# Performance work log

Hardware: AMD Instinct MI355X
Metric: run time of the kernel (lower is better)

The kernel has to match this reference:

```python
import jax, jax.numpy as jnp
import numpy as np
import math

B, N, C = 4, 8192, 384
H = 6
D = C // H  # head_dim = 64


def setup_inputs() -> dict:
    key = jax.random.key(0)
    ks = jax.random.split(key, 9)
    s = 1.0 / math.sqrt(D)
    x = jax.random.normal(ks[0], (B, N, C), dtype=jnp.float32)
    Wq = jax.random.normal(ks[1], (H, D, D), dtype=jnp.float32) * s
    bq = jax.random.normal(ks[2], (H, D), dtype=jnp.float32) * 0.01
    Wk = jax.random.normal(ks[3], (H, D, D), dtype=jnp.float32) * s
    bk = jax.random.normal(ks[4], (H, D), dtype=jnp.float32) * 0.01
    Wv = jax.random.normal(ks[5], (H, D, D), dtype=jnp.float32) * s
    bv = jax.random.normal(ks[6], (H, D), dtype=jnp.float32) * 0.01
    Wp = jax.random.normal(ks[7], (C, C), dtype=jnp.float32) * (1.0 / math.sqrt(C))
    bp = jax.random.normal(ks[8], (C,), dtype=jnp.float32) * 0.01
    return {"x": x, "Wq": Wq, "bq": bq, "Wk": Wk, "bk": bk,
            "Wv": Wv, "bv": bv, "Wp": Wp, "bp": bp}


def reference(x, Wq, bq, Wk, bk, Wv, bv, Wp, bp):
    b, n, c = x.shape
    # [B, H, N, D]
    xh = x.reshape(b, n, H, D).transpose(0, 2, 1, 3)
    # Batched per-head projections (replaces the Python loop of per-head Linears)
    q = jnp.einsum('bhnd,hde->bhne', xh, Wq) + bq[:, None, :]
    k = jnp.einsum('bhnd,hde->bhne', xh, Wk) + bk[:, None, :]
    v = jnp.einsum('bhnd,hde->bhne', xh, Wv) + bv[:, None, :]
    q = jax.nn.softmax(q, axis=-1)          # over feature dim
    k = jax.nn.softmax(k, axis=-2)          # over sequence dim
    v = v * (1.0 / math.sqrt(D))
    kv = jnp.einsum('bhnd,bhne->bhde', k, v)   # [B,H,D,D] context
    out = jnp.einsum('bhnd,bhde->bhne', q, kv) # [B,H,N,D]
    out = out.transpose(0, 2, 1, 3).reshape(b, n, c)
    return out @ Wp.T + bp
```

## Files before the change

### kernel.cpp

```cpp
#include <hip/hip_runtime.h>
#include <hip/hip_bf16.h>


#define B 4
#define N 8192
#define C 384
#define H 6
#define D 64
#define BH (B * H)
#define BN (B * N)

typedef __attribute__((ext_vector_type(8))) short short8;
typedef __attribute__((ext_vector_type(4))) float f32x4;

__device__ inline unsigned short f2bf(float f) {
    unsigned int u = __float_as_uint(f);
    unsigned int r = (u + 0x7fff + ((u >> 16) & 1)) >> 16;
    return (unsigned short)r;
}
__device__ inline float bf2f(unsigned short h) {
    return __uint_as_float(((unsigned int)h) << 16);
}

__global__ void wprep(const float* __restrict__ Wq, const float* __restrict__ Wk,
                      const float* __restrict__ Wv,
                      unsigned short* __restrict__ Whi, unsigned short* __restrict__ Wlo)
{
    __shared__ float tmp[64][65];
    const int m = blockIdx.x / H;
    const int h = blockIdx.x % H;
    const float* in = (m == 0 ? Wq : m == 1 ? Wk : Wv) + h * 64 * 64;
    const int t = threadIdx.x;
    for (int d = 0; d < 64; ++d) tmp[d][t] = in[d * 64 + t];
    __syncthreads();
    const size_t base = ((size_t)(m * H + h)) * 64 * 64;
    for (int e = 0; e < 64; ++e) {
        float v = tmp[t][e];
        unsigned short hb = f2bf(v);
        Whi[base + e * 64 + t] = hb;
        Wlo[base + e * 64 + t] = f2bf(v - bf2f(hb));
    }
}

__global__ __launch_bounds__(256, 2) void proj_kernel(
    const float* __restrict__ x,
    const unsigned short* __restrict__ Whi, const unsigned short* __restrict__ Wlo,
    const float* __restrict__ bq, const float* __restrict__ bk,
    const float* __restrict__ bv,
    unsigned short* __restrict__ qout,
    float* __restrict__ kvraw, float* __restrict__ Sg)
{
    __shared__ __align__(16) char smem[81920];
    float* A_s = (float*)smem;
    unsigned short* W_s = (unsigned short*)(smem + 17408);
    unsigned short* qbuf = (unsigned short*)(smem + 72704);
    float* kvred = (float*)smem;
    float* sred  = (float*)(smem + 67584);

    const int blk = blockIdx.x;
    const int nb  = blk & 31;
    const int bh  = blk >> 5;
    const int b   = bh / H;
    const int h   = bh % H;
    const int n0  = nb * 256;
    const int t   = threadIdx.x;
    const int lane = t & 63;
    const int w   = t >> 6;
    const int lq  = lane & 15;
    const int qd  = lane >> 4;

    {
        const size_t hb64 = (size_t)h * 64 * 64;
        for (int id = t; id < 512; id += 256) {
            int e = id >> 3, j = id & 7;
            #pragma unroll
            for (int m = 0; m < 3; ++m) {
                const size_t src = ((size_t)m * H) * 64 * 64 + hb64 + e * 64 + 8 * j;
                *(uint4*)&W_s[(2 * m) * 4608 + e * 72 + 8 * j] = *(const uint4*)(Whi + src);
                *(uint4*)&W_s[(2 * m + 1) * 4608 + e * 72 + 8 * j] = *(const uint4*)(Wlo + src);
            }
        }
    }

    float bqv[4], bkv[4], bvv[4];
    #pragma unroll
    for (int j = 0; j < 4; ++j) {
        int col = j * 16 + lq;
        bqv[j] = bq[h * D + col];
        bkv[j] = bk[h * D + col];
        bvv[j] = bv[h * D + col];
    }

    f32x4 kvacc[4][4] = {};
    float sacc[4] = {};

    for (int sub = 0; sub < 4; ++sub) {
        __syncthreads();
        const int ns = n0 + sub * 64;
        for (int id = t; id < 1024; id += 256) {
            int r = id >> 4, j = id & 15;
            *(float4*)&A_s[r * 68 + 4 * j] =
                *(const float4*)(x + (size_t)(b * N + ns + r) * C + h * D + 4 * j);
        }
        __syncthreads();

        f32x4 acc[3][4] = {};
        #pragma unroll
        for (int ck = 0; ck < 2; ++ck) {
            const float* ap = A_s + (w * 16 + lq) * 68 + ck * 32 + qd * 8;
            float av[8];
            *(float4*)&av[0] = *(const float4*)ap;
            *(float4*)&av[4] = *(const float4*)(ap + 4);
            short8 ahi, alo;
            #pragma unroll
            for (int i = 0; i < 8; ++i) {
                unsigned short hb = f2bf(av[i]);
                ahi[i] = (short)hb;
                alo[i] = (short)f2bf(av[i] - bf2f(hb));
            }
            #pragma unroll
            for (int m = 0; m < 3; ++m) {
                #pragma unroll
                for (int j = 0; j < 4; ++j) {
                    const unsigned short* bp =
                        W_s + (2 * m) * 4608 + (j * 16 + lq) * 72 + ck * 32 + qd * 8;
                    short8 bhi = *(const short8*)bp;
                    short8 blo = *(const short8*)(bp + 4608);
                    acc[m][j] = __builtin_amdgcn_mfma_f32_16x16x32_bf16(alo, bhi, acc[m][j], 0, 0, 0);
                    acc[m][j] = __builtin_amdgcn_mfma_f32_16x16x32_bf16(ahi, blo, acc[m][j], 0, 0, 0);
                    acc[m][j] = __builtin_amdgcn_mfma_f32_16x16x32_bf16(ahi, bhi, acc[m][j], 0, 0, 0);
                }
            }
        }

        #pragma unroll
        for (int r = 0; r < 4; ++r) {
            const int row = w * 16 + qd * 4 + r;
            float qv[4];
            #pragma unroll
            for (int j = 0; j < 4; ++j) qv[j] = acc[0][j][r] + bqv[j];
            float mx = fmaxf(fmaxf(qv[0], qv[1]), fmaxf(qv[2], qv[3]));
            #pragma unroll
            for (int msk = 1; msk < 16; msk <<= 1) mx = fmaxf(mx, __shfl_xor(mx, msk));
            float e0 = __expf(qv[0] - mx), e1 = __expf(qv[1] - mx);
            float e2 = __expf(qv[2] - mx), e3 = __expf(qv[3] - mx);
            float s = e0 + e1 + e2 + e3;
            #pragma unroll
            for (int msk = 1; msk < 16; msk <<= 1) s += __shfl_xor(s, msk);
            float inv = 1.f / s;
            qbuf[row * 72 + 0 * 16 + lq] = f2bf(e0 * inv);
            qbuf[row * 72 + 1 * 16 + lq] = f2bf(e1 * inv);
            qbuf[row * 72 + 2 * 16 + lq] = f2bf(e2 * inv);
            qbuf[row * 72 + 3 * 16 + lq] = f2bf(e3 * inv);
        }

        short8 kfrag[4], vfrag[4];
        #pragma unroll
        for (int j = 0; j < 4; ++j) {
            float e0 = __expf(acc[1][j][0] + bkv[j]);
            float e1 = __expf(acc[1][j][1] + bkv[j]);
            float e2 = __expf(acc[1][j][2] + bkv[j]);
            float e3 = __expf(acc[1][j][3] + bkv[j]);
            float cs = e0 + e1 + e2 + e3;
            cs += __shfl_xor(cs, 16);
            cs += __shfl_xor(cs, 32);
            sacc[j] += cs;
            kfrag[j] = short8{(short)f2bf(e0), (short)f2bf(e1),
                              (short)f2bf(e2), (short)f2bf(e3), 0, 0, 0, 0};
            float v0 = (acc[2][j][0] + bvv[j]) * 0.125f;
            float v1 = (acc[2][j][1] + bvv[j]) * 0.125f;
            float v2 = (acc[2][j][2] + bvv[j]) * 0.125f;
            float v3 = (acc[2][j][3] + bvv[j]) * 0.125f;
            vfrag[j] = short8{(short)f2bf(v0), (short)f2bf(v1),
                              (short)f2bf(v2), (short)f2bf(v3), 0, 0, 0, 0};
        }
        #pragma unroll
        for (int i = 0; i < 4; ++i)
            #pragma unroll
            for (int j = 0; j < 4; ++j)
                kvacc[i][j] = __builtin_amdgcn_mfma_f32_16x16x32_bf16(
                    kfrag[i], vfrag[j], kvacc[i][j], 0, 0, 0);

        __syncthreads();
        for (int id = t; id < 512; id += 256) {
            int r = id >> 3, j = id & 7;
            *(uint4*)&qout[((size_t)bh * N + ns + r) * D + 8 * j] =
                *(uint4*)&qbuf[r * 72 + 8 * j];
        }
    }

    __syncthreads();

    #pragma unroll
    for (int i = 0; i < 4; ++i)
        #pragma unroll
        for (int j = 0; j < 4; ++j)
            #pragma unroll
            for (int r = 0; r < 4; ++r)
                kvred[w * 4224 + (i * 16 + qd * 4 + r) * 66 + j * 16 + lq] =
                    kvacc[i][j][r];
    if (qd == 0) {
        #pragma unroll
        for (int j = 0; j < 4; ++j) sred[w * 64 + j * 16 + lq] = sacc[j];
    }
    __syncthreads();

    for (int idx = t; idx < 4096; idx += 256) {
        int d = idx >> 6, e = idx & 63;
        float s = kvred[d * 66 + e] + kvred[4224 + d * 66 + e]
                + kvred[2 * 4224 + d * 66 + e] + kvred[3 * 4224 + d * 66 + e];
        atomicAdd(&kvraw[bh * 4096 + idx], s);
    }
    if (t < 64) {
        float s = sred[t] + sred[64 + t] + sred[128 + t] + sred[192 + t];
        atomicAdd(&Sg[bh * 64 + t], s);
    }
}

__global__ __launch_bounds__(256) void kw_kernel(
    const float* __restrict__ kvraw, const float* __restrict__ Sg,
    const float* __restrict__ Wp, unsigned short* __restrict__ KWT)
{
    __shared__ float kv_s[64 * 68];
    __shared__ float w_s[64 * 68];
    __shared__ float rS_s[64];
    const int bh = blockIdx.x / (C / 64);
    const int ct = blockIdx.x % (C / 64);
    const int b = bh / H, h = bh % H;
    const int c0 = ct * 64;
    const int t = threadIdx.x, dg = t >> 4, cg = t & 15;

    if (t < 64) rS_s[t] = 1.f / Sg[bh * 64 + t];
    __syncthreads();

    for (int i = t; i < 4096; i += 256) {
        int row = i >> 6, e = i & 63;
        kv_s[e * 68 + row] = kvraw[bh * (D * D) + row * 64 + e] * rS_s[row];
        w_s[e * 68 + row]  = Wp[(size_t)(c0 + row) * C + h * 64 + e];
    }
    __syncthreads();

    float acc[4][4] = {};
    for (int e = 0; e < 64; ++e) {
        float4 a = *(float4*)&kv_s[e * 68 + dg * 4];
        float4 w = *(float4*)&w_s[e * 68 + cg * 4];
        const float a4[4] = {a.x, a.y, a.z, a.w};
        const float w4[4] = {w.x, w.y, w.z, w.w};
        #pragma unroll
        for (int i = 0; i < 4; ++i)
            #pragma unroll
            for (int j = 0; j < 4; ++j) acc[i][j] += a4[i] * w4[j];
    }
    #pragma unroll
    for (int i = 0; i < 4; ++i)
        #pragma unroll
        for (int j = 0; j < 4; ++j) {
            int d = dg * 4 + i, c = c0 + cg * 4 + j;
            KWT[((size_t)b * C + c) * (H * D) + h * 64 + d] = f2bf(acc[i][j]);
        }
}

__global__ __launch_bounds__(256) void out_gemm(
    const unsigned short* __restrict__ q, const unsigned short* __restrict__ KWT,
    const float* __restrict__ bp, float* __restrict__ out)
{
    __shared__ __align__(16) unsigned short A_s[128 * 72];
    __shared__ __align__(16) unsigned short B_s[128 * 72];

    const int mt = blockIdx.x / (C / 128);
    const int ct = blockIdx.x % (C / 128);
    const int m0 = mt * 128, c0 = ct * 128;
    const int b  = m0 >> 13;
    const int n0 = m0 & (N - 1);
    const int t  = threadIdx.x;
    const int lane = t & 63;
    const int w  = t >> 6;
    const int wm = w >> 1, wn = w & 1;
    const int lq = lane & 15;
    const int qd = lane >> 4;

    f32x4 acc[4][4] = {};

    for (int h = 0; h < H; ++h) {
        if (h) __syncthreads();
        const unsigned short* qb = q + (size_t)(b * H + h) * N * D + (size_t)n0 * D;
        const unsigned short* kb = KWT + ((size_t)b * C + c0) * (H * D) + h * 64;
        #pragma unroll
        for (int it = 0; it < 4; ++it) {
            int id = it * 256 + t;
            int r = id >> 3, c8 = id & 7;
            *(uint4*)&A_s[r * 72 + c8 * 8] = *(const uint4*)(qb + r * 64 + c8 * 8);
            *(uint4*)&B_s[r * 72 + c8 * 8] = *(const uint4*)(kb + (size_t)r * (H * D) + c8 * 8);
        }
        __syncthreads();

        #pragma unroll
        for (int kk = 0; kk < 64; kk += 32) {
            short8 af[4], bf[4];
            #pragma unroll
            for (int i = 0; i < 4; ++i)
                af[i] = *(short8*)&A_s[(wm * 64 + i * 16 + lq) * 72 + kk + qd * 8];
            #pragma unroll
            for (int j = 0; j < 4; ++j)
                bf[j] = *(short8*)&B_s[(wn * 64 + j * 16 + lq) * 72 + kk + qd * 8];
            #pragma unroll
            for (int i = 0; i < 4; ++i)
                #pragma unroll
                for (int j = 0; j < 4; ++j)
                    acc[i][j] = __builtin_amdgcn_mfma_f32_16x16x32_bf16(
                        af[i], bf[j], acc[i][j], 0, 0, 0);
        }
    }

    float bpv[4];
    #pragma unroll
    for (int j = 0; j < 4; ++j) bpv[j] = bp[c0 + wn * 64 + j * 16 + lq];

    #pragma unroll
    for (int i = 0; i < 4; ++i) {
        #pragma unroll
        for (int r = 0; r < 4; ++r) {
            size_t row = (size_t)m0 + wm * 64 + i * 16 + qd * 4 + r;
            float* orow = out + row * C + c0 + wn * 64;
            #pragma unroll
            for (int j = 0; j < 4; ++j)
                orow[j * 16 + lq] = acc[i][j][r] + bpv[j];
        }
    }
}

extern "C" void kernel_launch(void* const* d_in, const int* in_sizes, int n_in,
                              void* d_out, int out_size, void* d_ws, size_t ws_size,
                              hipStream_t stream)
{
    const float* x  = (const float*)d_in[0];
    const float* Wq = (const float*)d_in[1];
    const float* bq = (const float*)d_in[2];
    const float* Wk = (const float*)d_in[3];
    const float* bk = (const float*)d_in[4];
    const float* Wv = (const float*)d_in[5];
    const float* bv = (const float*)d_in[6];
    const float* Wp = (const float*)d_in[7];
    const float* bp = (const float*)d_in[8];
    float* out = (float*)d_out;

    const size_t SZ = (size_t)B * H * N * D;
    float* ws   = (float*)d_ws;
    unsigned short* q = (unsigned short*)ws;
    float* kvraw = ws + SZ;
    float* Sg    = kvraw + (size_t)BH * D * D;
    unsigned short* KWT = (unsigned short*)(Sg + BH * 64);
    unsigned short* Whi = KWT + (size_t)B * C * (H * D);
    unsigned short* Wlo = Whi + (size_t)3 * H * 64 * 64;

    wprep<<<3 * H, 64, 0, stream>>>(Wq, Wk, Wv, Whi, Wlo);
    hipMemsetAsync(kvraw, 0, ((size_t)BH * D * D + BH * 64) * sizeof(float), stream);
    proj_kernel<<<BH * (N / 256), 256, 0, stream>>>(x, Whi, Wlo, bq, bk, bv,
                                                    q, kvraw, Sg);
    kw_kernel<<<BH * (C / 64), 256, 0, stream>>>(kvraw, Sg, Wp, KWT);
    out_gemm<<<(BN / 128) * (C / 128), 256, 0, stream>>>(q, KWT, bp, out);
}
```

Baseline: 184.1 us.

## Cut proj_kernel LDS to fit three blocks per CU, prefetching x into registers

The projection kernel stops staging x through shared memory. Each lane now loads its A fragment straight from global memory, with the next sub-tile prefetched into registers, which removes two barriers per iteration. The weight tile uses an XOR-swizzled unpadded layout, q is written directly to global, and the kv reduction is split into two halves, so LDS drops to 48KB and launch bounds rise to 3 blocks per CU. The risks are register pressure under the tighter bound and uncoalesced 2-byte global stores for q.

Measured after the change: 339.3 us. 1.84x slower.

```diff
diff --git a/kernel.cpp b/kernel.cpp
--- a/kernel.cpp
+++ b/kernel.cpp
@@ -42,7 +42,7 @@
     }
 }
 
-__global__ __launch_bounds__(256, 2) void proj_kernel(
+__global__ __launch_bounds__(256, 3) void proj_kernel(
     const float* __restrict__ x,
     const unsigned short* __restrict__ Whi, const unsigned short* __restrict__ Wlo,
     const float* __restrict__ bq, const float* __restrict__ bk,
@@ -50,12 +50,10 @@
     unsigned short* __restrict__ qout,
     float* __restrict__ kvraw, float* __restrict__ Sg)
 {
-    __shared__ __align__(16) char smem[81920];
-    float* A_s = (float*)smem;
-    unsigned short* W_s = (unsigned short*)(smem + 17408);
-    unsigned short* qbuf = (unsigned short*)(smem + 72704);
+    __shared__ __align__(16) char smem[49152];
+    unsigned short* W_s = (unsigned short*)smem;
     float* kvred = (float*)smem;
-    float* sred  = (float*)(smem + 67584);
+    float* sred  = (float*)(smem + 33792);
 
     const int blk = blockIdx.x;
     const int nb  = blk & 31;
@@ -72,12 +70,13 @@
     {
         const size_t hb64 = (size_t)h * 64 * 64;
         for (int id = t; id < 512; id += 256) {
-            int e = id >> 3, j = id & 7;
+            int e = id >> 3, c = id & 7;
+            int dc = ((c ^ (e & 7)) * 8);
             #pragma unroll
             for (int m = 0; m < 3; ++m) {
-                const size_t src = ((size_t)m * H) * 64 * 64 + hb64 + e * 64 + 8 * j;
-                *(uint4*)&W_s[(2 * m) * 4608 + e * 72 + 8 * j] = *(const uint4*)(Whi + src);
-                *(uint4*)&W_s[(2 * m + 1) * 4608 + e * 72 + 8 * j] = *(const uint4*)(Wlo + src);
+                const size_t src = ((size_t)m * H) * 64 * 64 + hb64 + e * 64 + c * 8;
+                *(uint4*)&W_s[(2 * m) * 4096 + e * 64 + dc] = *(const uint4*)(Whi + src);
+                *(uint4*)&W_s[(2 * m + 1) * 4096 + e * 64 + dc] = *(const uint4*)(Wlo + src);
             }
         }
     }
@@ -91,51 +90,64 @@
         bvv[j] = bv[h * D + col];
     }
 
+    const float* xp = x + (size_t)(b * N + n0 + w * 16 + lq) * C + h * D + qd * 8;
+    const size_t xstep = (size_t)64 * C;
+
+    float4 cur0 = *(const float4*)xp;
+    float4 cur1 = *(const float4*)(xp + 4);
+    float4 cur2 = *(const float4*)(xp + 32);
+    float4 cur3 = *(const float4*)(xp + 36);
+
+    __syncthreads();
+
     f32x4 kvacc[4][4] = {};
     float sacc[4] = {};
 
     for (int sub = 0; sub < 4; ++sub) {
-        __syncthreads();
         const int ns = n0 + sub * 64;
-        for (int id = t; id < 1024; id += 256) {
-            int r = id >> 4, j = id & 15;
-            *(float4*)&A_s[r * 68 + 4 * j] =
-                *(const float4*)(x + (size_t)(b * N + ns + r) * C + h * D + 4 * j);
-        }
-        __syncthreads();
+        float4 nx0, nx1, nx2, nx3;
+        if (sub < 3) {
+            const float* np = xp + (sub + 1) * xstep;
+            nx0 = *(const float4*)np;
+            nx1 = *(const float4*)(np + 4);
+            nx2 = *(const float4*)(np + 32);
+            nx3 = *(const float4*)(np + 36);
+        }
+
+        float av[16];
+        *(float4*)&av[0]  = cur0; *(float4*)&av[4]  = cur1;
+        *(float4*)&av[8]  = cur2; *(float4*)&av[12] = cur3;
+        short8 ahi[2], alo[2];
+        #pragma unroll
+        for (int ck = 0; ck < 2; ++ck)
+            #pragma unroll
+            for (int i = 0; i < 8; ++i) {
+                float v = av[ck * 8 + i];
+                unsigned short hb = f2bf(v);
+                ahi[ck][i] = (short)hb;
+                alo[ck][i] = (short)f2bf(v - bf2f(hb));
+            }
 
         f32x4 acc[3][4] = {};
         #pragma unroll
         for (int ck = 0; ck < 2; ++ck) {
-            const float* ap = A_s + (w * 16 + lq) * 68 + ck * 32 + qd * 8;
-            float av[8];
-            *(float4*)&av[0] = *(const float4*)ap;
-            *(float4*)&av[4] = *(const float4*)(ap + 4);
-            short8 ahi, alo;
-            #pragma unroll
-            for (int i = 0; i < 8; ++i) {
-                unsigned short hb = f2bf(av[i]);
-                ahi[i] = (short)hb;
-                alo[i] = (short)f2bf(av[i] - bf2f(hb));
-            }
             #pragma unroll
             for (int m = 0; m < 3; ++m) {
                 #pragma unroll
                 for (int j = 0; j < 4; ++j) {
-                    const unsigned short* bp =
-                        W_s + (2 * m) * 4608 + (j * 16 + lq) * 72 + ck * 32 + qd * 8;
-                    short8 bhi = *(const short8*)bp;
-                    short8 blo = *(const short8*)(bp + 4608);
-                    acc[m][j] = __builtin_amdgcn_mfma_f32_16x16x32_bf16(alo, bhi, acc[m][j], 0, 0, 0);
-                    acc[m][j] = __builtin_amdgcn_mfma_f32_16x16x32_bf16(ahi, blo, acc[m][j], 0, 0, 0);
-                    acc[m][j] = __builtin_amdgcn_mfma_f32_16x16x32_bf16(ahi, bhi, acc[m][j], 0, 0, 0);
+                    const int row = j * 16 + lq;
+                    const int pc = ((ck * 4 + qd) ^ (lq & 7)) * 8;
+                    short8 bhi = *(const short8*)&W_s[(2 * m) * 4096 + row * 64 + pc];
+                    short8 blo = *(const short8*)&W_s[(2 * m + 1) * 4096 + row * 64 + pc];
+                    acc[m][j] = __builtin_amdgcn_mfma_f32_16x16x32_bf16(alo[ck], bhi, acc[m][j], 0, 0, 0);
+                    acc[m][j] = __builtin_amdgcn_mfma_f32_16x16x32_bf16(ahi[ck], blo, acc[m][j], 0, 0, 0);
+                    acc[m][j] = __builtin_amdgcn_mfma_f32_16x16x32_bf16(ahi[ck], bhi, acc[m][j], 0, 0, 0);
                 }
             }
         }
 
         #pragma unroll
         for (int r = 0; r < 4; ++r) {
-            const int row = w * 16 + qd * 4 + r;
             float qv[4];
             #pragma unroll
             for (int j = 0; j < 4; ++j) qv[j] = acc[0][j][r] + bqv[j];
@@ -148,10 +160,12 @@
             #pragma unroll
             for (int msk = 1; msk < 16; msk <<= 1) s += __shfl_xor(s, msk);
             float inv = 1.f / s;
-            qbuf[row * 72 + 0 * 16 + lq] = f2bf(e0 * inv);
-            qbuf[row * 72 + 1 * 16 + lq] = f2bf(e1 * inv);
-            qbuf[row * 72 + 2 * 16 + lq] = f2bf(e2 * inv);
-            qbuf[row * 72 + 3 * 16 + lq] = f2bf(e3 * inv);
+            unsigned short* qr =
+                qout + ((size_t)bh * N + ns + w * 16 + qd * 4 + r) * 64 + lq;
+            qr[0]  = f2bf(e0 * inv);
+            qr[16] = f2bf(e1 * inv);
+            qr[32] = f2bf(e2 * inv);
+            qr[48] = f2bf(e3 * inv);
         }
 
         short8 kfrag[4], vfrag[4];
@@ -181,39 +195,39 @@
                 kvacc[i][j] = __builtin_amdgcn_mfma_f32_16x16x32_bf16(
                     kfrag[i], vfrag[j], kvacc[i][j], 0, 0, 0);
 
+        cur0 = nx0; cur1 = nx1; cur2 = nx2; cur3 = nx3;
+    }
+
+    __syncthreads();
+
+    #pragma unroll
+    for (int half = 0; half < 2; ++half) {
+        #pragma unroll
+        for (int i2 = 0; i2 < 2; ++i2) {
+            const int ii = half * 2 + i2;
+            #pragma unroll
+            for (int j = 0; j < 4; ++j)
+                #pragma unroll
+                for (int r = 0; r < 4; ++r)
+                    kvred[w * 2112 + (i2 * 16 + qd * 4 + r) * 66 + j * 16 + lq] =
+                        kvacc[ii][j][r];
+        }
+        if (half == 0 && qd == 0) {
+            #pragma unroll
+            for (int j = 0; j < 4; ++j) sred[w * 64 + j * 16 + lq] = sacc[j];
+        }
         __syncthreads();
-        for (int id = t; id < 512; id += 256) {
-            int r = id >> 3, j = id & 7;
-            *(uint4*)&qout[((size_t)bh * N + ns + r) * D + 8 * j] =
-                *(uint4*)&qbuf[r * 72 + 8 * j];
-        }
-    }
-
-    __syncthreads();
-
-    #pragma unroll
-    for (int i = 0; i < 4; ++i)
-        #pragma unroll
-        for (int j = 0; j < 4; ++j)
-            #pragma unroll
-            for (int r = 0; r < 4; ++r)
-                kvred[w * 4224 + (i * 16 + qd * 4 + r) * 66 + j * 16 + lq] =
-                    kvacc[i][j][r];
-    if (qd == 0) {
-        #pragma unroll
-        for (int j = 0; j < 4; ++j) sred[w * 64 + j * 16 + lq] = sacc[j];
-    }
-    __syncthreads();
-
-    for (int idx = t; idx < 4096; idx += 256) {
-        int d = idx >> 6, e = idx & 63;
-        float s = kvred[d * 66 + e] + kvred[4224 + d * 66 + e]
-                + kvred[2 * 4224 + d * 66 + e] + kvred[3 * 4224 + d * 66 + e];
-        atomicAdd(&kvraw[bh * 4096 + idx], s);
-    }
-    if (t < 64) {
-        float s = sred[t] + sred[64 + t] + sred[128 + t] + sred[192 + t];
-        atomicAdd(&Sg[bh * 64 + t], s);
+        for (int idx = t; idx < 2048; idx += 256) {
+            int dl = idx >> 6, e = idx & 63;
+            float s = kvred[dl * 66 + e] + kvred[2112 + dl * 66 + e]
+                    + kvred[2 * 2112 + dl * 66 + e] + kvred[3 * 2112 + dl * 66 + e];
+            atomicAdd(&kvraw[bh * 4096 + (half * 32 + dl) * 64 + e], s);
+        }
+        if (half == 1 && t < 64) {
+            float s = sred[t] + sred[64 + t] + sred[128 + t] + sred[192 + t];
+            atomicAdd(&Sg[bh * 64 + t], s);
+        }
+        if (half == 0) __syncthreads();
     }
 }
 
```
